# Kernel tuning notes

Hardware: AMD Instinct MI355X
Metric: run time of the kernel (lower is better)

## Reference

```python
import jax, jax.numpy as jnp
import numpy as np

D_MODEL = 1024
D_STATE = 16
BATCH = 4
SEQLEN = 4096


def setup_inputs() -> dict:
    key = jax.random.key(0)
    kx, kA, kB, kC = jax.random.split(key, 4)
    x = jax.random.normal(kx, (BATCH, SEQLEN, D_MODEL), dtype=jnp.float32)
    # Params per init_weights(): A ~ N(-0.5, 0.1), B ~ N(0, 0.1), C ~ N(0, 0.1), D = 0
    A = -0.5 + 0.1 * jax.random.normal(kA, (1, D_STATE), dtype=jnp.float32)
    B_in = 0.1 * jax.random.normal(kB, (D_MODEL, D_STATE), dtype=jnp.float32)
    C = 0.1 * jax.random.normal(kC, (D_STATE, D_MODEL), dtype=jnp.float32)
    D = jnp.zeros((D_MODEL,), dtype=jnp.float32)
    return {"x": x, "A": A, "B_in": B_in, "C": C, "D": D}


def reference(x, A, B_in, C, D):
    # x: [B, N, E]; A: [1, S]; B_in: [E, S]; C: [S, E]; D: [E]
    A_neg = -jnp.exp(A)                              # [1, S]
    Bx = jnp.einsum('bne,es->bns', x, B_in)          # [B, N, S] = x @ B
    delta = jax.nn.softplus(Bx)                      # softplus(u @ B)
    decay = jnp.exp(delta * A_neg)                   # [B, N, S]

    def step(h, inp):
        d_t, bx_t = inp                              # each [B, S]
        h = h * d_t + bx_t
        return h, h

    h0 = jnp.zeros((x.shape[0], A.shape[1]), dtype=x.dtype)
    # scan over time: inputs [N, B, S]
    _, hs = jax.lax.scan(step, h0, (decay.transpose(1, 0, 2), Bx.transpose(1, 0, 2)))
    # readout: y_t = h_t @ C + x_t * D  (dropout p=0.0 -> identity)
    y = jnp.einsum('nbs,se->bne', hs, C) + x * D
    return y
```

## Files before the change

kernel.cpp:

```cpp
#include <hip/hip_runtime.h>

#define NSEQ 4096
#define EDIM 1024

#define OFF_PBX  0u
#define OFF_HLOC 1048576u
#define OFF_PINC 1310720u
#define OFF_SUM  1572864u

__device__ __forceinline__ void fma4(float4& a, float xv, const float4& b) {
    a.x = fmaf(xv, b.x, a.x);
    a.y = fmaf(xv, b.y, a.y);
    a.z = fmaf(xv, b.z, a.z);
    a.w = fmaf(xv, b.w, a.w);
}

__global__ __launch_bounds__(256, 4) void k1_bx(const float* __restrict__ x,
                                                const float* __restrict__ Bin,
                                                float* __restrict__ ws) {
    __shared__ __align__(16) float smem[2 * 64 * 68];
    const int tid  = threadIdx.x;
    const int lane = tid & 63;
    const int wu   = __builtin_amdgcn_readfirstlane(tid) >> 6;
    const int q    = blockIdx.x & 3;
    const int r0   = (blockIdx.x >> 2) * 64;
    const int b    = r0 >> 12;
    const int n0   = r0 & 4095;
    const int eq   = q * 256;

    const float4* xf4 = (const float4*)x;
    const float4* Bf4 = (const float4*)Bin;

    float acc[16];
#pragma unroll
    for (int s = 0; s < 16; s++) acc[s] = 0.f;

    float4 pf[4];
#pragma unroll
    for (int k = 0; k < 4; k++) {
        int i = tid + 256 * k, row = i >> 4, cq = i & 15;
        pf[k] = xf4[(size_t)(r0 + row) * 256 + q * 64 + cq];
    }
#pragma unroll
    for (int k = 0; k < 4; k++) {
        int i = tid + 256 * k, row = i >> 4, cq = i & 15;
        *(float4*)&smem[row * 68 + cq * 4] = pf[k];
    }
    __syncthreads();

    for (int c = 0; c < 4; ++c) {
        if (c < 3) {
#pragma unroll
            for (int k = 0; k < 4; k++) {
                int i = tid + 256 * k, row = i >> 4, cq = i & 15;
                pf[k] = xf4[(size_t)(r0 + row) * 256 + q * 64 + (c + 1) * 16 + cq];
            }
        }
        const float* stg = &smem[(c & 1) * 4352];
#pragma unroll
        for (int jj = 0; jj < 4; ++jj) {
            const float4 xq = *(const float4*)&stg[lane * 68 + wu * 16 + jj * 4];
            const float xs[4] = {xq.x, xq.y, xq.z, xq.w};
#pragma unroll
            for (int m = 0; m < 4; ++m) {
                const int e = eq + c * 64 + wu * 16 + jj * 4 + m;
                const float4 b0 = Bf4[e * 4 + 0];
                const float4 b1 = Bf4[e * 4 + 1];
                const float4 b2 = Bf4[e * 4 + 2];
                const float4 b3 = Bf4[e * 4 + 3];
                const float xv = xs[m];
                acc[0]  = fmaf(xv, b0.x, acc[0]);  acc[1]  = fmaf(xv, b0.y, acc[1]);
                acc[2]  = fmaf(xv, b0.z, acc[2]);  acc[3]  = fmaf(xv, b0.w, acc[3]);
                acc[4]  = fmaf(xv, b1.x, acc[4]);  acc[5]  = fmaf(xv, b1.y, acc[5]);
                acc[6]  = fmaf(xv, b1.z, acc[6]);  acc[7]  = fmaf(xv, b1.w, acc[7]);
                acc[8]  = fmaf(xv, b2.x, acc[8]);  acc[9]  = fmaf(xv, b2.y, acc[9]);
                acc[10] = fmaf(xv, b2.z, acc[10]); acc[11] = fmaf(xv, b2.w, acc[11]);
                acc[12] = fmaf(xv, b3.x, acc[12]); acc[13] = fmaf(xv, b3.y, acc[13]);
                acc[14] = fmaf(xv, b3.z, acc[14]); acc[15] = fmaf(xv, b3.w, acc[15]);
            }
        }
        if (c < 3) {
            float* dst = &smem[((c + 1) & 1) * 4352];
#pragma unroll
            for (int k = 0; k < 4; k++) {
                int i = tid + 256 * k, row = i >> 4, cq = i & 15;
                *(float4*)&dst[row * 68 + cq * 4] = pf[k];
            }
        }
        __syncthreads();
    }

    {
        const int rb = (wu * 64 + lane) * 17;
#pragma unroll
        for (int s = 0; s < 16; s++) smem[rb + s] = acc[s];
    }
    __syncthreads();

#pragma unroll
    for (int p = 0; p < 4; p++) {
        const int o   = tid + 256 * p;
        const int s   = o >> 6;
        const int row = o & 63;
        const float v = smem[(0 * 64 + row) * 17 + s] + smem[(1 * 64 + row) * 17 + s] +
                        smem[(2 * 64 + row) * 17 + s] + smem[(3 * 64 + row) * 17 + s];
        ws[OFF_PBX + (size_t)q * 262144u + (size_t)(b * 16 + s) * NSEQ + n0 + row] = v;
    }
}

__global__ __launch_bounds__(256) void k2_scan(const float* __restrict__ A,
                                               float* __restrict__ ws) {
    __shared__ float sP[4], sH[4];
    const int tid   = threadIdx.x;
    const int lane  = tid & 63;
    const int w     = tid >> 6;
    const int chain = blockIdx.x >> 4;
    const int chunk = blockIdx.x & 15;
    const int ss    = chain & 15;
    const int t     = chunk * 256 + tid;

    float bxv = 0.f;
#pragma unroll
    for (int q = 0; q < 4; q++)
        bxv += ws[OFF_PBX + (size_t)q * 262144u + (size_t)chain * NSEQ + t];

    const float Ae = expf(A[ss]);
    const float sp = fmaxf(bxv, 0.f) + log1pf(expf(-fabsf(bxv)));
    const float de = expf(-Ae * sp);

    float Pi = de, hi = bxv;
#pragma unroll
    for (int off = 1; off < 64; off <<= 1) {
        float Pp = __shfl_up(Pi, off, 64);
        float hp = __shfl_up(hi, off, 64);
        if (lane >= off) { hi = fmaf(hp, Pi, hi); Pi *= Pp; }
    }
    if (lane == 63) { sP[w] = Pi; sH[w] = hi; }
    __syncthreads();
    float Hw = 0.f, Pw = 1.f;
    for (int qq = 0; qq < w; qq++) { Hw = fmaf(Hw, sP[qq], sH[qq]); Pw *= sP[qq]; }

    const float hloc = fmaf(Hw, Pi, hi);
    const float pinc = Pw * Pi;
    ws[OFF_HLOC + (size_t)chain * NSEQ + t] = hloc;
    ws[OFF_PINC + (size_t)chain * NSEQ + t] = pinc;
    if (tid == 255) {
        ws[OFF_SUM + (chain * 16 + chunk) * 2 + 0] = pinc;
        ws[OFF_SUM + (chain * 16 + chunk) * 2 + 1] = hloc;
    }
}

__global__ __launch_bounds__(256) void k3_out(const float* __restrict__ x,
                                              const float* __restrict__ C,
                                              const float* __restrict__ D,
                                              const float* __restrict__ ws,
                                              float* __restrict__ out) {
    __shared__ float sh[16 * 17];
    const int tid = threadIdx.x;
    const int blk = blockIdx.x;
    const int tc  = blk & 255;
    const int b   = blk >> 8;
    const int t0  = tc * 16;
    const int chunk = t0 >> 8;

    {
        const int s  = tid >> 4;
        const int tt = tid & 15;
        const int chain = b * 16 + s;
        float H = 0.f;
        for (int c = 0; c < chunk; ++c) {
            const float Pc = ws[OFF_SUM + (chain * 16 + c) * 2 + 0];
            const float hc = ws[OFF_SUM + (chain * 16 + c) * 2 + 1];
            H = fmaf(H, Pc, hc);
        }
        const int t = t0 + tt;
        const float h = fmaf(ws[OFF_PINC + (size_t)chain * NSEQ + t], H,
                             ws[OFF_HLOC + (size_t)chain * NSEQ + t]);
        sh[tt * 17 + s] = h;
    }

    const float4* C4 = (const float4*)C;
    float4 creg[16];
#pragma unroll
    for (int s = 0; s < 16; s++) creg[s] = C4[s * 256 + tid];
    const float4 dreg = ((const float4*)D)[tid];
    const bool needX = __any((dreg.x != 0.f) | (dreg.y != 0.f) |
                             (dreg.z != 0.f) | (dreg.w != 0.f));
    __syncthreads();

    const float4* x4 = (const float4*)x;
    float4* o4 = (float4*)out;
    const size_t rowbase = ((size_t)b * NSEQ + t0) * 256;

    if (needX) {
#pragma unroll 4
        for (int tt = 0; tt < 16; tt++) {
            float4 xv = x4[rowbase + tt * 256 + tid];
            float4 y;
            y.x = xv.x * dreg.x; y.y = xv.y * dreg.y;
            y.z = xv.z * dreg.z; y.w = xv.w * dreg.w;
#pragma unroll
            for (int s = 0; s < 16; s++) fma4(y, sh[tt * 17 + s], creg[s]);
            o4[rowbase + tt * 256 + tid] = y;
        }
    } else {
#pragma unroll 4
        for (int tt = 0; tt < 16; tt++) {
            float4 y = make_float4(0.f, 0.f, 0.f, 0.f);
#pragma unroll
            for (int s = 0; s < 16; s++) fma4(y, sh[tt * 17 + s], creg[s]);
            o4[rowbase + tt * 256 + tid] = y;
        }
    }
}

extern "C" void kernel_launch(void* const* d_in, const int* in_sizes, int n_in,
                              void* d_out, int out_size, void* d_ws, size_t ws_size,
                              hipStream_t stream) {
    const float* x   = (const float*)d_in[0];
    const float* A   = (const float*)d_in[1];
    const float* Bin = (const float*)d_in[2];
    const float* C   = (const float*)d_in[3];
    const float* D   = (const float*)d_in[4];
    float* out = (float*)d_out;
    float* ws  = (float*)d_ws;

    hipLaunchKernelGGL(k1_bx,   dim3(1024), dim3(256), 0, stream, x, Bin, ws);
    hipLaunchKernelGGL(k2_scan, dim3(1024), dim3(256), 0, stream, A, ws);
    hipLaunchKernelGGL(k3_out,  dim3(1024), dim3(256), 0, stream, x, C, D, ws, out);
}
```

Before: 147.2 us.

## Fuse Bx projection with local chunk scan and add separate carry kernel

The Bx projection kernel now has each block cover the full embedding dimension for 64 rows, so no partial sums go to global memory. The same kernel then computes softplus and decay and runs a per-chunk warp scan, writing (h, P) pairs. A small carry kernel scans the 64 chunk summaries per chain, so the output kernel no longer loops over earlier chunks. This removes the partial-Bx round trip and one launch's worth of traffic, but grid size drops from 1024 to 256 blocks, each with a longer serial K loop, which reduces parallelism in the first kernel.

Measured after the change: 186.3 us. 1.27x slower.

```diff
diff --git a/kernel.cpp b/kernel.cpp
--- a/kernel.cpp
+++ b/kernel.cpp
@@ -3,10 +3,9 @@
 #define NSEQ 4096
 #define EDIM 1024
 
-#define OFF_PBX  0u
-#define OFF_HLOC 1048576u
-#define OFF_PINC 1310720u
-#define OFF_SUM  1572864u
+#define OFF_HP  0u
+#define OFF_SUM 524288u
+#define OFF_H0  532480u
 
 __device__ __forceinline__ void fma4(float4& a, float xv, const float4& b) {
     a.x = fmaf(xv, b.x, a.x);
@@ -15,18 +14,17 @@
     a.w = fmaf(xv, b.w, a.w);
 }
 
-__global__ __launch_bounds__(256, 4) void k1_bx(const float* __restrict__ x,
-                                                const float* __restrict__ Bin,
-                                                float* __restrict__ ws) {
+__global__ __launch_bounds__(256) void k1_bxscan(const float* __restrict__ x,
+                                                 const float* __restrict__ A,
+                                                 const float* __restrict__ Bin,
+                                                 float* __restrict__ ws) {
     __shared__ __align__(16) float smem[2 * 64 * 68];
     const int tid  = threadIdx.x;
     const int lane = tid & 63;
     const int wu   = __builtin_amdgcn_readfirstlane(tid) >> 6;
-    const int q    = blockIdx.x & 3;
-    const int r0   = (blockIdx.x >> 2) * 64;
+    const int r0   = blockIdx.x * 64;
     const int b    = r0 >> 12;
     const int n0   = r0 & 4095;
-    const int eq   = q * 256;
 
     const float4* xf4 = (const float4*)x;
     const float4* Bf4 = (const float4*)Bin;
@@ -35,35 +33,32 @@
 #pragma unroll
     for (int s = 0; s < 16; s++) acc[s] = 0.f;
 
-    float4 pf[4];
+    float4 pfA[4], pfB[4];
 #pragma unroll
     for (int k = 0; k < 4; k++) {
         int i = tid + 256 * k, row = i >> 4, cq = i & 15;
-        pf[k] = xf4[(size_t)(r0 + row) * 256 + q * 64 + cq];
+        pfA[k] = xf4[(size_t)(r0 + row) * 256 + cq];
     }
 #pragma unroll
     for (int k = 0; k < 4; k++) {
         int i = tid + 256 * k, row = i >> 4, cq = i & 15;
-        *(float4*)&smem[row * 68 + cq * 4] = pf[k];
+        *(float4*)&smem[row * 68 + cq * 4] = pfA[k];
     }
     __syncthreads();
-
-    for (int c = 0; c < 4; ++c) {
-        if (c < 3) {
-#pragma unroll
-            for (int k = 0; k < 4; k++) {
-                int i = tid + 256 * k, row = i >> 4, cq = i & 15;
-                pf[k] = xf4[(size_t)(r0 + row) * 256 + q * 64 + (c + 1) * 16 + cq];
-            }
-        }
-        const float* stg = &smem[(c & 1) * 4352];
+#pragma unroll
+    for (int k = 0; k < 4; k++) {
+        int i = tid + 256 * k, row = i >> 4, cq = i & 15;
+        pfA[k] = xf4[(size_t)(r0 + row) * 256 + 16 + cq];
+    }
+
+    auto compute = [&](int c, const float* stg) {
 #pragma unroll
         for (int jj = 0; jj < 4; ++jj) {
             const float4 xq = *(const float4*)&stg[lane * 68 + wu * 16 + jj * 4];
             const float xs[4] = {xq.x, xq.y, xq.z, xq.w};
 #pragma unroll
             for (int m = 0; m < 4; ++m) {
-                const int e = eq + c * 64 + wu * 16 + jj * 4 + m;
+                const int e = c * 64 + wu * 16 + jj * 4 + m;
                 const float4 b0 = Bf4[e * 4 + 0];
                 const float4 b1 = Bf4[e * 4 + 1];
                 const float4 b2 = Bf4[e * 4 + 2];
@@ -79,12 +74,38 @@
                 acc[14] = fmaf(xv, b3.z, acc[14]); acc[15] = fmaf(xv, b3.w, acc[15]);
             }
         }
-        if (c < 3) {
-            float* dst = &smem[((c + 1) & 1) * 4352];
-#pragma unroll
-            for (int k = 0; k < 4; k++) {
-                int i = tid + 256 * k, row = i >> 4, cq = i & 15;
-                *(float4*)&dst[row * 68 + cq * 4] = pf[k];
+    };
+
+    for (int c = 0; c < 16; c += 2) {
+        if (c + 2 < 16) {
+#pragma unroll
+            for (int k = 0; k < 4; k++) {
+                int i = tid + 256 * k, row = i >> 4, cq = i & 15;
+                pfB[k] = xf4[(size_t)(r0 + row) * 256 + (c + 2) * 16 + cq];
+            }
+        }
+        compute(c, &smem[0]);
+        {
+#pragma unroll
+            for (int k = 0; k < 4; k++) {
+                int i = tid + 256 * k, row = i >> 4, cq = i & 15;
+                *(float4*)&smem[4352 + row * 68 + cq * 4] = pfA[k];
+            }
+        }
+        __syncthreads();
+        if (c + 3 < 16) {
+#pragma unroll
+            for (int k = 0; k < 4; k++) {
+                int i = tid + 256 * k, row = i >> 4, cq = i & 15;
+                pfA[k] = xf4[(size_t)(r0 + row) * 256 + (c + 3) * 16 + cq];
+            }
+        }
+        compute(c + 1, &smem[4352]);
+        if (c + 2 < 16) {
+#pragma unroll
+            for (int k = 0; k < 4; k++) {
+                int i = tid + 256 * k, row = i >> 4, cq = i & 15;
+                *(float4*)&smem[row * 68 + cq * 4] = pfB[k];
             }
         }
         __syncthreads();
@@ -97,57 +118,44 @@
     }
     __syncthreads();
 
-#pragma unroll
-    for (int p = 0; p < 4; p++) {
-        const int o   = tid + 256 * p;
-        const int s   = o >> 6;
-        const int row = o & 63;
-        const float v = smem[(0 * 64 + row) * 17 + s] + smem[(1 * 64 + row) * 17 + s] +
-                        smem[(2 * 64 + row) * 17 + s] + smem[(3 * 64 + row) * 17 + s];
-        ws[OFF_PBX + (size_t)q * 262144u + (size_t)(b * 16 + s) * NSEQ + n0 + row] = v;
-    }
-}
-
-__global__ __launch_bounds__(256) void k2_scan(const float* __restrict__ A,
-                                               float* __restrict__ ws) {
-    __shared__ float sP[4], sH[4];
-    const int tid   = threadIdx.x;
-    const int lane  = tid & 63;
-    const int w     = tid >> 6;
-    const int chain = blockIdx.x >> 4;
-    const int chunk = blockIdx.x & 15;
-    const int ss    = chain & 15;
-    const int t     = chunk * 256 + tid;
-
-    float bxv = 0.f;
-#pragma unroll
-    for (int q = 0; q < 4; q++)
-        bxv += ws[OFF_PBX + (size_t)q * 262144u + (size_t)chain * NSEQ + t];
-
-    const float Ae = expf(A[ss]);
-    const float sp = fmaxf(bxv, 0.f) + log1pf(expf(-fabsf(bxv)));
-    const float de = expf(-Ae * sp);
-
-    float Pi = de, hi = bxv;
+    const int chunk = n0 >> 6;
+    float2* HP = (float2*)(ws + OFF_HP);
+    float2* SU = (float2*)(ws + OFF_SUM);
+#pragma unroll
+    for (int j = 0; j < 4; ++j) {
+        const int s = wu * 4 + j;
+        const float bx = smem[lane * 17 + s] + smem[(64 + lane) * 17 + s] +
+                         smem[(128 + lane) * 17 + s] + smem[(192 + lane) * 17 + s];
+        const float Ae = expf(A[s]);
+        const float sp = fmaxf(bx, 0.f) + log1pf(expf(-fabsf(bx)));
+        const float de = expf(-Ae * sp);
+        float Pi = de, hi = bx;
+#pragma unroll
+        for (int off = 1; off < 64; off <<= 1) {
+            float Pp = __shfl_up(Pi, off, 64);
+            float hp = __shfl_up(hi, off, 64);
+            if (lane >= off) { hi = fmaf(hp, Pi, hi); Pi *= Pp; }
+        }
+        const int chain = b * 16 + s;
+        HP[(size_t)chain * NSEQ + n0 + lane] = make_float2(hi, Pi);
+        if (lane == 63) SU[chain * 64 + chunk] = make_float2(hi, Pi);
+    }
+}
+
+__global__ __launch_bounds__(64) void k2_carry(float* __restrict__ ws) {
+    const int chain = blockIdx.x;
+    const int lane  = threadIdx.x;
+    const float2 sv = ((const float2*)(ws + OFF_SUM))[chain * 64 + lane];
+    float hi = sv.x, Pi = sv.y;
 #pragma unroll
     for (int off = 1; off < 64; off <<= 1) {
         float Pp = __shfl_up(Pi, off, 64);
         float hp = __shfl_up(hi, off, 64);
         if (lane >= off) { hi = fmaf(hp, Pi, hi); Pi *= Pp; }
     }
-    if (lane == 63) { sP[w] = Pi; sH[w] = hi; }
-    __syncthreads();
-    float Hw = 0.f, Pw = 1.f;
-    for (int qq = 0; qq < w; qq++) { Hw = fmaf(Hw, sP[qq], sH[qq]); Pw *= sP[qq]; }
-
-    const float hloc = fmaf(Hw, Pi, hi);
-    const float pinc = Pw * Pi;
-    ws[OFF_HLOC + (size_t)chain * NSEQ + t] = hloc;
-    ws[OFF_PINC + (size_t)chain * NSEQ + t] = pinc;
-    if (tid == 255) {
-        ws[OFF_SUM + (chain * 16 + chunk) * 2 + 0] = pinc;
-        ws[OFF_SUM + (chain * 16 + chunk) * 2 + 1] = hloc;
-    }
+    float He = __shfl_up(hi, 1, 64);
+    if (lane == 0) He = 0.f;
+    ws[OFF_H0 + chain * 64 + lane] = He;
 }
 
 __global__ __launch_bounds__(256) void k3_out(const float* __restrict__ x,
@@ -161,22 +169,15 @@
     const int tc  = blk & 255;
     const int b   = blk >> 8;
     const int t0  = tc * 16;
-    const int chunk = t0 >> 8;
 
     {
         const int s  = tid >> 4;
         const int tt = tid & 15;
         const int chain = b * 16 + s;
-        float H = 0.f;
-        for (int c = 0; c < chunk; ++c) {
-            const float Pc = ws[OFF_SUM + (chain * 16 + c) * 2 + 0];
-            const float hc = ws[OFF_SUM + (chain * 16 + c) * 2 + 1];
-            H = fmaf(H, Pc, hc);
-        }
         const int t = t0 + tt;
-        const float h = fmaf(ws[OFF_PINC + (size_t)chain * NSEQ + t], H,
-                             ws[OFF_HLOC + (size_t)chain * NSEQ + t]);
-        sh[tt * 17 + s] = h;
+        const float2 hp = ((const float2*)(ws + OFF_HP))[(size_t)chain * NSEQ + t];
+        const float h0  = ws[OFF_H0 + chain * 64 + (t >> 6)];
+        sh[tt * 17 + s] = fmaf(hp.y, h0, hp.x);
     }
 
     const float4* C4 = (const float4*)C;
@@ -225,7 +226,7 @@
     float* out = (float*)d_out;
     float* ws  = (float*)d_ws;
 
-    hipLaunchKernelGGL(k1_bx,   dim3(1024), dim3(256), 0, stream, x, Bin, ws);
-    hipLaunchKernelGGL(k2_scan, dim3(1024), dim3(256), 0, stream, A, ws);
-    hipLaunchKernelGGL(k3_out,  dim3(1024), dim3(256), 0, stream, x, C, D, ws, out);
-}
+    hipLaunchKernelGGL(k1_bxscan, dim3(256),  dim3(256), 0, stream, x, A, Bin, ws);
+    hipLaunchKernelGGL(k2_carry,  dim3(64),   dim3(64),  0, stream, ws);
+    hipLaunchKernelGGL(k3_out,    dim3(1024), dim3(256), 0, stream, x, C, D, ws, out);
+}
```
